# Performance work log

Hardware: AMD Instinct MI355X
Metric: run time of the kernel (lower is better)

The kernel has to match this reference:

```python
import jax, jax.numpy as jnp
import numpy as np

SCALE_POS = 2.0
SCALE_NEG = 40.0
THRESH_POS = 0.5
THRESH_NEG = 0.5
MARGIN = 0.1
EPS = 1e-5


def setup_inputs() -> dict:
    key = jax.random.key(0)
    kf, kl = jax.random.split(key)
    B, D, NUM_CLASSES = 4096, 1024, 64
    feats = jax.random.normal(kf, (B, D), dtype=jnp.float32)
    feats = feats / jnp.linalg.norm(feats, axis=1, keepdims=True)  # L2-normalized embeddings
    labels = jax.random.randint(kl, (B,), 0, NUM_CLASSES, dtype=jnp.int64)
    return {"feats": feats, "labels": labels}


def reference(feats, labels):
    B = feats.shape[0]
    sim = jnp.matmul(feats, feats.T)  # [B, B]
    same = labels[:, None] == labels[None, :]
    pos_mask = same & (sim < 1.0 - EPS)  # drop self / near-duplicate pairs
    neg_mask = ~same

    # hard mining: keep negatives above min positive - margin, positives below max negative + margin
    min_pos = jnp.min(jnp.where(pos_mask, sim, jnp.inf), axis=1)   # [B]
    max_neg = jnp.max(jnp.where(neg_mask, sim, -jnp.inf), axis=1)  # [B]
    neg_sel = neg_mask & (sim + MARGIN > min_pos[:, None])
    pos_sel = pos_mask & (sim - MARGIN < max_neg[:, None])

    pos_sum = jnp.sum(jnp.where(pos_sel, jnp.exp(-SCALE_POS * (sim - THRESH_POS)), 0.0), axis=1)
    neg_sum = jnp.sum(jnp.where(neg_sel, jnp.exp(SCALE_NEG * (sim - THRESH_NEG)), 0.0), axis=1)
    pos_loss = jnp.log1p(pos_sum) / SCALE_POS
    neg_loss = jnp.log1p(neg_sum) / SCALE_NEG

    valid = jnp.any(pos_sel, axis=1) & jnp.any(neg_sel, axis=1)  # rows skipped by original loop
    return jnp.sum(jnp.where(valid, pos_loss + neg_loss, 0.0)) / B
```

## Files before the change

kernel.cpp:

```cpp
#include <hip/hip_runtime.h>

typedef _Float16 half8 __attribute__((ext_vector_type(8)));
typedef float floatx4 __attribute__((ext_vector_type(4)));
typedef int intx4 __attribute__((ext_vector_type(4)));
typedef int intx8 __attribute__((ext_vector_type(8)));
typedef __attribute__((address_space(1))) const void gvoid;
typedef __attribute__((address_space(3))) void svoid;

#define SCALE_POS 2.0f
#define SCALE_NEG 40.0f
#define THRESH 0.5f
#define MARGIN 0.1f
#define EPSV 1e-5f

__global__ void k_init(const float* __restrict__ feats,
                       unsigned char* __restrict__ f8,
                       float* __restrict__ out,
                       int total4) {
    int i = blockIdx.x * blockDim.x + threadIdx.x;
    if (i < total4) {
        float4 v = ((const float4*)feats)[i];
        int w = 0;
        w = __builtin_amdgcn_cvt_pk_fp8_f32(v.x, v.y, w, false);
        w = __builtin_amdgcn_cvt_pk_fp8_f32(v.z, v.w, w, true);
        ((int*)f8)[i] = w;
    }
    if (i == 0) out[0] = 0.f;
}

__global__ void __launch_bounds__(256, 4)
k_gemm_h(const unsigned char* __restrict__ f8,
         const int* __restrict__ labels,
         float* __restrict__ pmin,
         float* __restrict__ pmax,
         _Float16* __restrict__ simh,
         int D, int nb) {
    __shared__ __align__(16) unsigned char As[128 * 128];
    __shared__ __align__(16) unsigned char Bs[128 * 128];
    __shared__ int labR[128], labC[128];

    const int Bsz = nb * 128;

    const int bid0 = blockIdx.x;
    const int t = (bid0 & 7) * 66 + (bid0 >> 3);
    int rb = 0, rem = t;
    while (rem >= nb - rb) { rem -= nb - rb; ++rb; }
    const int cb = rb + rem;
    const int rowBase = rb * 128;
    const int colBase = cb * 128;

    const int tid = threadIdx.x;
    const int lane = tid & 63;
    const int wave = tid >> 6;
    const int wr = wave >> 1;
    const int wc = wave & 1;
    const int q = lane >> 4;
    const int cIn = lane & 15;

    if (tid < 128) labR[tid] = labels[rowBase + tid];
    else           labC[tid - 128] = labels[colBase + (tid - 128)];

    const int subrow = lane >> 3;
    const int swz = (lane & 7) ^ subrow;
    const unsigned char* gP[8];
    unsigned char* lP[8];
#pragma unroll
    for (int j = 0; j < 8; ++j) {
        const int c = wave * 8 + j;
        const int grow = (c < 16) ? (rowBase + c * 8 + subrow)
                                  : (colBase + (c - 16) * 8 + subrow);
        gP[j] = f8 + (size_t)grow * D + swz * 16;
        lP[j] = ((c < 16) ? (As + c * 1024) : (Bs + (c - 16) * 1024)) + lane * 16;
    }

    int aOff0[4], aOff1[4], bOff0[4], bOff1[4];
#pragma unroll
    for (int i = 0; i < 4; ++i) {
        const int rA = wr * 64 + i * 16 + cIn;
        aOff0[i] = rA * 128 + ((2 * q) ^ (rA & 7)) * 16;
        aOff1[i] = rA * 128 + ((2 * q + 1) ^ (rA & 7)) * 16;
        const int rB = wc * 64 + i * 16 + cIn;
        bOff0[i] = rB * 128 + ((2 * q) ^ (rB & 7)) * 16;
        bOff1[i] = rB * 128 + ((2 * q + 1) ^ (rB & 7)) * 16;
    }

    floatx4 acc[4][4] = {};

    const int KT = D >> 7;
    for (int kt = 0; kt < KT; ++kt) {
        const int kOff = kt * 128;
        __syncthreads();
#pragma unroll
        for (int j = 0; j < 8; ++j)
            __builtin_amdgcn_global_load_lds((gvoid*)(gP[j] + kOff), (svoid*)lP[j], 16, 0, 0);
        __syncthreads();

        intx8 a[4], b[4];
#pragma unroll
        for (int i = 0; i < 4; ++i) {
            intx4 lo = *(const intx4*)(As + aOff0[i]);
            intx4 hi = *(const intx4*)(As + aOff1[i]);
            a[i] = __builtin_shufflevector(lo, hi, 0, 1, 2, 3, 4, 5, 6, 7);
        }
#pragma unroll
        for (int i = 0; i < 4; ++i) {
            intx4 lo = *(const intx4*)(Bs + bOff0[i]);
            intx4 hi = *(const intx4*)(Bs + bOff1[i]);
            b[i] = __builtin_shufflevector(lo, hi, 0, 1, 2, 3, 4, 5, 6, 7);
        }
#pragma unroll
        for (int i = 0; i < 4; ++i)
#pragma unroll
            for (int j2 = 0; j2 < 4; ++j2)
                acc[i][j2] = __builtin_amdgcn_mfma_scale_f32_16x16x128_f8f6f4(
                    a[i], b[j2], acc[i][j2], 0, 0,
                    0, 0x7f7f7f7f,
                    0, 0x7f7f7f7f);
    }

    int rLabv[16];
#pragma unroll
    for (int mi = 0; mi < 4; ++mi)
#pragma unroll
        for (int rr = 0; rr < 4; ++rr)
            rLabv[mi * 4 + rr] = labR[wr * 64 + mi * 16 + q * 4 + rr];
    int cLabv[4];
#pragma unroll
    for (int ni = 0; ni < 4; ++ni)
        cLabv[ni] = labC[wc * 64 + ni * 16 + cIn];

    {
        half8* dst = (half8*)(simh + (size_t)(2 * t + wc) * 8192
                                   + (size_t)(wr * 64 + lane) * 64);
#pragma unroll
        for (int mi = 0; mi < 4; ++mi) {
            half8 h0, h1;
#pragma unroll
            for (int ni = 0; ni < 2; ++ni)
#pragma unroll
                for (int rr = 0; rr < 4; ++rr) {
                    h0[ni * 4 + rr] = (_Float16)acc[mi][ni][rr];
                    h1[ni * 4 + rr] = (_Float16)acc[mi][ni + 2][rr];
                }
            dst[mi * 2] = h0;
            dst[mi * 2 + 1] = h1;
        }
    }

    {
        float* pmnRow = pmin + (size_t)(2 * cb + wc) * Bsz + rowBase;
        float* pmxRow = pmax + (size_t)(2 * cb + wc) * Bsz + rowBase;
#pragma unroll
        for (int mi = 0; mi < 4; ++mi)
#pragma unroll
            for (int rr = 0; rr < 4; ++rr) {
                const int rLoc = wr * 64 + mi * 16 + q * 4 + rr;
                const int rLab = rLabv[mi * 4 + rr];
                float vmin = 1e30f, vmax = -1e30f;
#pragma unroll
                for (int ni = 0; ni < 4; ++ni) {
                    float s = acc[mi][ni][rr];
                    if (rLab == cLabv[ni]) {
                        if (s < 1.0f - EPSV) vmin = fminf(vmin, s);
                    } else {
                        vmax = fmaxf(vmax, s);
                    }
                }
#pragma unroll
                for (int off = 8; off; off >>= 1) {
                    vmin = fminf(vmin, __shfl_xor(vmin, off, 16));
                    vmax = fmaxf(vmax, __shfl_xor(vmax, off, 16));
                }
                if (cIn == 0) {
                    pmnRow[rLoc] = vmin;
                    pmxRow[rLoc] = vmax;
                }
            }
    }

    if (rb != cb) {
        float* pmnCol = pmin + (size_t)(2 * rb + wr) * Bsz + colBase;
        float* pmxCol = pmax + (size_t)(2 * rb + wr) * Bsz + colBase;
#pragma unroll
        for (int ni = 0; ni < 4; ++ni) {
            const int cLab = cLabv[ni];
            float vmin = 1e30f, vmax = -1e30f;
#pragma unroll
            for (int mi = 0; mi < 4; ++mi)
#pragma unroll
                for (int rr = 0; rr < 4; ++rr) {
                    float s = acc[mi][ni][rr];
                    if (rLabv[mi * 4 + rr] == cLab) {
                        if (s < 1.0f - EPSV) vmin = fminf(vmin, s);
                    } else {
                        vmax = fmaxf(vmax, s);
                    }
                }
            vmin = fminf(vmin, __shfl_xor(vmin, 16, 64));
            vmin = fminf(vmin, __shfl_xor(vmin, 32, 64));
            vmax = fmaxf(vmax, __shfl_xor(vmax, 16, 64));
            vmax = fmaxf(vmax, __shfl_xor(vmax, 32, 64));
            if (q == 0) {
                const int cLoc = wc * 64 + ni * 16 + cIn;
                pmnCol[cLoc] = vmin;
                pmxCol[cLoc] = vmax;
            }
        }
    }
}

__global__ void __launch_bounds__(256)
k_sum2f(const _Float16* __restrict__ simh,
        const int* __restrict__ labels,
        const float* __restrict__ pmin,
        const float* __restrict__ pmax,
        float* __restrict__ psP, float* __restrict__ psN,
        int nb, int B) {
    __shared__ int labR[128], labC[128];
    __shared__ float gNR[128], gPR[128], gNC[128], gPC[128];

    int t = blockIdx.x;
    int rb = 0, rem = t;
    while (rem >= nb - rb) { rem -= nb - rb; ++rb; }
    const int cb = rb + rem;
    const int rowBase = rb * 128;

    const int tid = threadIdx.x;
    const int sub = tid >> 7;
    const int stid = tid & 127;
    const int wave = stid >> 6;
    const int lane = tid & 63;
    const int q = lane >> 4;
    const int cIn = lane & 15;
    const int colBase = cb * 128 + sub * 64;

    {
        const int j = tid & 127;
        const int base = (tid < 128) ? (rowBase + j) : (cb * 128 + j);
        float mn = 1e30f, mx = -1e30f;
#pragma unroll 4
        for (int k = 0; k < 64; ++k) {
            mn = fminf(mn, pmin[(size_t)k * B + base]);
            mx = fmaxf(mx, pmax[(size_t)k * B + base]);
        }
        if (tid < 128) {
            labR[j] = labels[rowBase + j];
            gNR[j] = mn - MARGIN;
            gPR[j] = mx + MARGIN;
        } else {
            labC[j] = labels[cb * 128 + j];
            gNC[j] = mn - MARGIN;
            gPC[j] = mx + MARGIN;
        }
    }
    __syncthreads();

    int cLabv[4];
    float gNCv[4], gPCv[4];
#pragma unroll
    for (int ni = 0; ni < 4; ++ni) {
        const int j = sub * 64 + ni * 16 + cIn;
        cLabv[ni] = labC[j];
        gNCv[ni] = gNC[j];
        gPCv[ni] = gPC[j];
    }

    const half8* src = (const half8*)(simh + (size_t)(2 * t + sub) * 8192 + (size_t)stid * 64);
    half8 hv[8];
#pragma unroll
    for (int v = 0; v < 8; ++v) hv[v] = src[v];

    float cps[4] = {}, cns[4] = {};
    const bool offd = (rb != cb);

    float* psPRow = psP + (size_t)(2 * cb + sub) * B + rowBase;
    float* psNRow = psN + (size_t)(2 * cb + sub) * B + rowBase;

#pragma unroll
    for (int mi = 0; mi < 4; ++mi)
#pragma unroll
        for (int rr = 0; rr < 4; ++rr) {
            const int rLoc = wave * 64 + mi * 16 + q * 4 + rr;
            const int rLab = labR[rLoc];
            const float gn = gNR[rLoc];
            const float gp = gPR[rLoc];
            float rp = 0.f, rn = 0.f;
#pragma unroll
            for (int ni = 0; ni < 4; ++ni) {
                const int idx = mi * 16 + ni * 4 + rr;
                const float s = (float)hv[idx >> 3][idx & 7];
                if (rLab == cLabv[ni]) {
                    if (s < 1.0f - EPSV) {
                        float ev = __expf(-SCALE_POS * (s - THRESH));
                        if (s < gp) rp += ev;
                        if (offd && s < gPCv[ni]) cps[ni] += ev;
                    }
                } else {
                    float ev = __expf(SCALE_NEG * (s - THRESH));
                    if (s > gn) rn += ev;
                    if (offd && s > gNCv[ni]) cns[ni] += ev;
                }
            }
#pragma unroll
            for (int off = 8; off; off >>= 1) {
                rp += __shfl_xor(rp, off, 16);
                rn += __shfl_xor(rn, off, 16);
            }
            if (cIn == 0) {
                psPRow[rLoc] = rp;
                psNRow[rLoc] = rn;
            }
        }
    if (offd) {
        float* psPCol = psP + (size_t)(2 * rb + wave) * B + colBase;
        float* psNCol = psN + (size_t)(2 * rb + wave) * B + colBase;
#pragma unroll
        for (int ni = 0; ni < 4; ++ni) {
            cps[ni] += __shfl_xor(cps[ni], 16, 64);
            cps[ni] += __shfl_xor(cps[ni], 32, 64);
            cns[ni] += __shfl_xor(cns[ni], 16, 64);
            cns[ni] += __shfl_xor(cns[ni], 32, 64);
            if (q == 0) {
                const int cLoc = ni * 16 + cIn;
                psPCol[cLoc] = cps[ni];
                psNCol[cLoc] = cns[ni];
            }
        }
    }
}

__global__ void __launch_bounds__(256)
k_final(const float* __restrict__ psP, const float* __restrict__ psN,
        float* __restrict__ out, int B) {
    __shared__ float red[4];
    const int r = blockIdx.x * 256 + threadIdx.x;
    float P = 0.f, N = 0.f;
    for (int k = 0; k < 64; ++k) {
        P += psP[(size_t)k * B + r];
        N += psN[(size_t)k * B + r];
    }
    float a = (P > 0.f && N > 0.f)
                  ? log1pf(P) * (1.0f / SCALE_POS) + log1pf(N) * (1.0f / SCALE_NEG)
                  : 0.f;
#pragma unroll
    for (int off = 32; off; off >>= 1) a += __shfl_down(a, off, 64);
    const int tid = threadIdx.x;
    if ((tid & 63) == 0) red[tid >> 6] = a;
    __syncthreads();
    if (tid == 0)
        atomicAdd(out, (red[0] + red[1] + red[2] + red[3]) / (float)B);
}

extern "C" void kernel_launch(void* const* d_in, const int* in_sizes, int n_in,
                              void* d_out, int out_size, void* d_ws, size_t ws_size,
                              hipStream_t stream) {
    const float* feats = (const float*)d_in[0];
    const int* labels = (const int*)d_in[1];
    const int B = in_sizes[1];
    const int D = in_sizes[0] / B;
    const int nb = B / 128;
    const int NT = nb * (nb + 1) / 2;
    const int total4 = B * D / 4;

    char* ws = (char*)d_ws;
    unsigned char* f8 = (unsigned char*)ws;
    size_t off = (size_t)B * D;
    float* pmin = (float*)(ws + off); off += (size_t)64 * B * 4;
    float* pmax = (float*)(ws + off); off += (size_t)64 * B * 4;
    float* psP  = (float*)(ws + off); off += (size_t)64 * B * 4;
    float* psN  = (float*)(ws + off); off += (size_t)64 * B * 4;
    _Float16* simh = (_Float16*)(ws + ((off + 255) & ~(size_t)255));
    float* outp = (float*)d_out;

    k_init<<<(total4 + 255) / 256, 256, 0, stream>>>(feats, f8, outp, total4);

    k_gemm_h<<<NT, 256, 0, stream>>>(f8, labels, pmin, pmax, simh, D, nb);

    k_sum2f<<<NT, 256, 0, stream>>>(simh, labels, pmin, pmax, psP, psN, nb, B);

    k_final<<<B / 256, 256, 0, stream>>>(psP, psN, outp, B);
}
```

Baseline: 134.7 us.

## Split GEMM tile across eight waves with 64x32 per-wave subtiles

The similarity GEMM block grows from four to eight waves, so each wave computes a 64x32 subtile instead of 64x64, halving accumulator registers and per-wave global-to-LDS loads. This aims to hide more latency through more concurrent waves. The partial min/max buffers double to 128 slices to match the finer column split. Because column-direction stats fill only some slots, k_init now pre-fills the buffers with sentinel values. The cost is extra init writes and twice as many partial reads in the reduction kernel.

Result: no change. 136.6 us (+1.4%).

```diff
diff --git a/kernel.cpp b/kernel.cpp
--- a/kernel.cpp
+++ b/kernel.cpp
@@ -15,8 +15,9 @@
 
 __global__ void k_init(const float* __restrict__ feats,
                        unsigned char* __restrict__ f8,
+                       float* __restrict__ pmin, float* __restrict__ pmax,
                        float* __restrict__ out,
-                       int total4) {
+                       int total4, int nstat) {
     int i = blockIdx.x * blockDim.x + threadIdx.x;
     if (i < total4) {
         float4 v = ((const float4*)feats)[i];
@@ -25,10 +26,14 @@
         w = __builtin_amdgcn_cvt_pk_fp8_f32(v.z, v.w, w, true);
         ((int*)f8)[i] = w;
     }
+    if (i < nstat) {
+        pmin[i] = 1e30f;
+        pmax[i] = -1e30f;
+    }
     if (i == 0) out[0] = 0.f;
 }
 
-__global__ void __launch_bounds__(256, 4)
+__global__ void __launch_bounds__(512, 4)
 k_gemm_h(const unsigned char* __restrict__ f8,
          const int* __restrict__ labels,
          float* __restrict__ pmin,
@@ -52,50 +57,53 @@
     const int tid = threadIdx.x;
     const int lane = tid & 63;
     const int wave = tid >> 6;
-    const int wr = wave >> 1;
-    const int wc = wave & 1;
+    const int wr = wave >> 2;
+    const int wc4 = wave & 3;
     const int q = lane >> 4;
     const int cIn = lane & 15;
 
     if (tid < 128) labR[tid] = labels[rowBase + tid];
-    else           labC[tid - 128] = labels[colBase + (tid - 128)];
+    else if (tid < 256) labC[tid - 128] = labels[colBase + (tid - 128)];
 
     const int subrow = lane >> 3;
     const int swz = (lane & 7) ^ subrow;
-    const unsigned char* gP[8];
-    unsigned char* lP[8];
-#pragma unroll
-    for (int j = 0; j < 8; ++j) {
-        const int c = wave * 8 + j;
+    const unsigned char* gP[4];
+    unsigned char* lP[4];
+#pragma unroll
+    for (int j = 0; j < 4; ++j) {
+        const int c = wave * 4 + j;
         const int grow = (c < 16) ? (rowBase + c * 8 + subrow)
                                   : (colBase + (c - 16) * 8 + subrow);
         gP[j] = f8 + (size_t)grow * D + swz * 16;
         lP[j] = ((c < 16) ? (As + c * 1024) : (Bs + (c - 16) * 1024)) + lane * 16;
     }
 
-    int aOff0[4], aOff1[4], bOff0[4], bOff1[4];
+    int aOff0[4], aOff1[4], bOff0[2], bOff1[2];
 #pragma unroll
     for (int i = 0; i < 4; ++i) {
         const int rA = wr * 64 + i * 16 + cIn;
         aOff0[i] = rA * 128 + ((2 * q) ^ (rA & 7)) * 16;
         aOff1[i] = rA * 128 + ((2 * q + 1) ^ (rA & 7)) * 16;
-        const int rB = wc * 64 + i * 16 + cIn;
+    }
+#pragma unroll
+    for (int i = 0; i < 2; ++i) {
+        const int rB = wc4 * 32 + i * 16 + cIn;
         bOff0[i] = rB * 128 + ((2 * q) ^ (rB & 7)) * 16;
         bOff1[i] = rB * 128 + ((2 * q + 1) ^ (rB & 7)) * 16;
     }
 
-    floatx4 acc[4][4] = {};
+    floatx4 acc[4][2] = {};
 
     const int KT = D >> 7;
     for (int kt = 0; kt < KT; ++kt) {
         const int kOff = kt * 128;
         __syncthreads();
 #pragma unroll
-        for (int j = 0; j < 8; ++j)
+        for (int j = 0; j < 4; ++j)
             __builtin_amdgcn_global_load_lds((gvoid*)(gP[j] + kOff), (svoid*)lP[j], 16, 0, 0);
         __syncthreads();
 
-        intx8 a[4], b[4];
+        intx8 a[4], b[2];
 #pragma unroll
         for (int i = 0; i < 4; ++i) {
             intx4 lo = *(const intx4*)(As + aOff0[i]);
@@ -103,7 +111,7 @@
             a[i] = __builtin_shufflevector(lo, hi, 0, 1, 2, 3, 4, 5, 6, 7);
         }
 #pragma unroll
-        for (int i = 0; i < 4; ++i) {
+        for (int i = 0; i < 2; ++i) {
             intx4 lo = *(const intx4*)(Bs + bOff0[i]);
             intx4 hi = *(const intx4*)(Bs + bOff1[i]);
             b[i] = __builtin_shufflevector(lo, hi, 0, 1, 2, 3, 4, 5, 6, 7);
@@ -111,7 +119,7 @@
 #pragma unroll
         for (int i = 0; i < 4; ++i)
 #pragma unroll
-            for (int j2 = 0; j2 < 4; ++j2)
+            for (int j2 = 0; j2 < 2; ++j2)
                 acc[i][j2] = __builtin_amdgcn_mfma_scale_f32_16x16x128_f8f6f4(
                     a[i], b[j2], acc[i][j2], 0, 0,
                     0, 0x7f7f7f7f,
@@ -124,32 +132,29 @@
 #pragma unroll
         for (int rr = 0; rr < 4; ++rr)
             rLabv[mi * 4 + rr] = labR[wr * 64 + mi * 16 + q * 4 + rr];
-    int cLabv[4];
-#pragma unroll
-    for (int ni = 0; ni < 4; ++ni)
-        cLabv[ni] = labC[wc * 64 + ni * 16 + cIn];
+    int cLabv[2];
+#pragma unroll
+    for (int ni = 0; ni < 2; ++ni)
+        cLabv[ni] = labC[wc4 * 32 + ni * 16 + cIn];
 
     {
-        half8* dst = (half8*)(simh + (size_t)(2 * t + wc) * 8192
+        half8* dst = (half8*)(simh + (size_t)(2 * t + (wc4 >> 1)) * 8192
                                    + (size_t)(wr * 64 + lane) * 64);
 #pragma unroll
         for (int mi = 0; mi < 4; ++mi) {
-            half8 h0, h1;
+            half8 h0;
 #pragma unroll
             for (int ni = 0; ni < 2; ++ni)
 #pragma unroll
-                for (int rr = 0; rr < 4; ++rr) {
+                for (int rr = 0; rr < 4; ++rr)
                     h0[ni * 4 + rr] = (_Float16)acc[mi][ni][rr];
-                    h1[ni * 4 + rr] = (_Float16)acc[mi][ni + 2][rr];
-                }
-            dst[mi * 2] = h0;
-            dst[mi * 2 + 1] = h1;
+            dst[mi * 2 + (wc4 & 1)] = h0;
         }
     }
 
     {
-        float* pmnRow = pmin + (size_t)(2 * cb + wc) * Bsz + rowBase;
-        float* pmxRow = pmax + (size_t)(2 * cb + wc) * Bsz + rowBase;
+        float* pmnRow = pmin + (size_t)(4 * cb + wc4) * Bsz + rowBase;
+        float* pmxRow = pmax + (size_t)(4 * cb + wc4) * Bsz + rowBase;
 #pragma unroll
         for (int mi = 0; mi < 4; ++mi)
 #pragma unroll
@@ -158,7 +163,7 @@
                 const int rLab = rLabv[mi * 4 + rr];
                 float vmin = 1e30f, vmax = -1e30f;
 #pragma unroll
-                for (int ni = 0; ni < 4; ++ni) {
+                for (int ni = 0; ni < 2; ++ni) {
                     float s = acc[mi][ni][rr];
                     if (rLab == cLabv[ni]) {
                         if (s < 1.0f - EPSV) vmin = fminf(vmin, s);
@@ -179,10 +184,10 @@
     }
 
     if (rb != cb) {
-        float* pmnCol = pmin + (size_t)(2 * rb + wr) * Bsz + colBase;
-        float* pmxCol = pmax + (size_t)(2 * rb + wr) * Bsz + colBase;
-#pragma unroll
-        for (int ni = 0; ni < 4; ++ni) {
+        float* pmnCol = pmin + (size_t)(4 * rb + wr) * Bsz + colBase;
+        float* pmxCol = pmax + (size_t)(4 * rb + wr) * Bsz + colBase;
+#pragma unroll
+        for (int ni = 0; ni < 2; ++ni) {
             const int cLab = cLabv[ni];
             float vmin = 1e30f, vmax = -1e30f;
 #pragma unroll
@@ -201,7 +206,7 @@
             vmax = fmaxf(vmax, __shfl_xor(vmax, 16, 64));
             vmax = fmaxf(vmax, __shfl_xor(vmax, 32, 64));
             if (q == 0) {
-                const int cLoc = wc * 64 + ni * 16 + cIn;
+                const int cLoc = wc4 * 32 + ni * 16 + cIn;
                 pmnCol[cLoc] = vmin;
                 pmxCol[cLoc] = vmax;
             }
@@ -239,7 +244,7 @@
         const int base = (tid < 128) ? (rowBase + j) : (cb * 128 + j);
         float mn = 1e30f, mx = -1e30f;
 #pragma unroll 4
-        for (int k = 0; k < 64; ++k) {
+        for (int k = 0; k < 128; ++k) {
             mn = fminf(mn, pmin[(size_t)k * B + base]);
             mx = fmaxf(mx, pmax[(size_t)k * B + base]);
         }
@@ -361,20 +366,22 @@
     const int nb = B / 128;
     const int NT = nb * (nb + 1) / 2;
     const int total4 = B * D / 4;
+    const int nstat = 128 * B;
 
     char* ws = (char*)d_ws;
     unsigned char* f8 = (unsigned char*)ws;
     size_t off = (size_t)B * D;
-    float* pmin = (float*)(ws + off); off += (size_t)64 * B * 4;
-    float* pmax = (float*)(ws + off); off += (size_t)64 * B * 4;
+    float* pmin = (float*)(ws + off); off += (size_t)128 * B * 4;
+    float* pmax = (float*)(ws + off); off += (size_t)128 * B * 4;
     float* psP  = (float*)(ws + off); off += (size_t)64 * B * 4;
     float* psN  = (float*)(ws + off); off += (size_t)64 * B * 4;
     _Float16* simh = (_Float16*)(ws + ((off + 255) & ~(size_t)255));
     float* outp = (float*)d_out;
 
-    k_init<<<(total4 + 255) / 256, 256, 0, stream>>>(feats, f8, outp, total4);
-
-    k_gemm_h<<<NT, 256, 0, stream>>>(f8, labels, pmin, pmax, simh, D, nb);
+    k_init<<<(total4 + 255) / 256, 256, 0, stream>>>(feats, f8, pmin, pmax,
+                                                     outp, total4, nstat);
+
+    k_gemm_h<<<NT, 512, 0, stream>>>(f8, labels, pmin, pmax, simh, D, nb);
 
     k_sum2f<<<NT, 256, 0, stream>>>(simh, labels, pmin, pmax, psP, psN, nb, B);
 
```

## Fuse fp32-to-fp8 conversion into GEMM tile loads, drop init kernel

Applied to the files above, without the earlier changes.

Removes the separate conversion kernel. The GEMM now reads fp32 features directly, converts them to fp8 in registers and writes them into swizzled LDS, and zeroing the output moves into block 0. This drops a launch and the fp8 round trip through global memory. In exchange every tile reads 4x more bytes from global memory and loses the async global-to-LDS path, and launch bounds change from 4 to 2 waves per SIMD.

New measurement: 165.8 us. +23.1%, slower.

```diff
diff --git a/kernel.cpp b/kernel.cpp
--- a/kernel.cpp
+++ b/kernel.cpp
@@ -4,8 +4,6 @@
 typedef float floatx4 __attribute__((ext_vector_type(4)));
 typedef int intx4 __attribute__((ext_vector_type(4)));
 typedef int intx8 __attribute__((ext_vector_type(8)));
-typedef __attribute__((address_space(1))) const void gvoid;
-typedef __attribute__((address_space(3))) void svoid;
 
 #define SCALE_POS 2.0f
 #define SCALE_NEG 40.0f
@@ -13,27 +11,13 @@
 #define MARGIN 0.1f
 #define EPSV 1e-5f
 
-__global__ void k_init(const float* __restrict__ feats,
-                       unsigned char* __restrict__ f8,
-                       float* __restrict__ out,
-                       int total4) {
-    int i = blockIdx.x * blockDim.x + threadIdx.x;
-    if (i < total4) {
-        float4 v = ((const float4*)feats)[i];
-        int w = 0;
-        w = __builtin_amdgcn_cvt_pk_fp8_f32(v.x, v.y, w, false);
-        w = __builtin_amdgcn_cvt_pk_fp8_f32(v.z, v.w, w, true);
-        ((int*)f8)[i] = w;
-    }
-    if (i == 0) out[0] = 0.f;
-}
-
-__global__ void __launch_bounds__(256, 4)
-k_gemm_h(const unsigned char* __restrict__ f8,
+__global__ void __launch_bounds__(256, 2)
+k_gemm_h(const float* __restrict__ feats,
          const int* __restrict__ labels,
          float* __restrict__ pmin,
          float* __restrict__ pmax,
          _Float16* __restrict__ simh,
+         float* __restrict__ out,
          int D, int nb) {
     __shared__ __align__(16) unsigned char As[128 * 128];
     __shared__ __align__(16) unsigned char Bs[128 * 128];
@@ -57,20 +41,22 @@
     const int q = lane >> 4;
     const int cIn = lane & 15;
 
+    if (bid0 == 0 && tid == 0) out[0] = 0.f;
+
     if (tid < 128) labR[tid] = labels[rowBase + tid];
     else           labC[tid - 128] = labels[colBase + (tid - 128)];
 
     const int subrow = lane >> 3;
-    const int swz = (lane & 7) ^ subrow;
-    const unsigned char* gP[8];
-    unsigned char* lP[8];
+    const int blk = lane & 7;
+    const float* gF[8];
+    int wOff[8];
 #pragma unroll
     for (int j = 0; j < 8; ++j) {
         const int c = wave * 8 + j;
         const int grow = (c < 16) ? (rowBase + c * 8 + subrow)
                                   : (colBase + (c - 16) * 8 + subrow);
-        gP[j] = f8 + (size_t)grow * D + swz * 16;
-        lP[j] = ((c < 16) ? (As + c * 1024) : (Bs + (c - 16) * 1024)) + lane * 16;
+        gF[j] = feats + (size_t)grow * D + blk * 16;
+        wOff[j] = c * 1024 + subrow * 128 + ((blk ^ subrow) << 4);
     }
 
     int aOff0[4], aOff1[4], bOff0[4], bOff1[4];
@@ -88,11 +74,23 @@
 
     const int KT = D >> 7;
     for (int kt = 0; kt < KT; ++kt) {
-        const int kOff = kt * 128;
         __syncthreads();
 #pragma unroll
-        for (int j = 0; j < 8; ++j)
-            __builtin_amdgcn_global_load_lds((gvoid*)(gP[j] + kOff), (svoid*)lP[j], 16, 0, 0);
+        for (int j = 0; j < 8; ++j) {
+            const floatx4* sp = (const floatx4*)(gF[j] + kt * 128);
+            floatx4 f0 = sp[0], f1 = sp[1], f2 = sp[2], f3 = sp[3];
+            int w0 = 0, w1 = 0, w2 = 0, w3 = 0;
+            w0 = __builtin_amdgcn_cvt_pk_fp8_f32(f0[0], f0[1], w0, false);
+            w0 = __builtin_amdgcn_cvt_pk_fp8_f32(f0[2], f0[3], w0, true);
+            w1 = __builtin_amdgcn_cvt_pk_fp8_f32(f1[0], f1[1], w1, false);
+            w1 = __builtin_amdgcn_cvt_pk_fp8_f32(f1[2], f1[3], w1, true);
+            w2 = __builtin_amdgcn_cvt_pk_fp8_f32(f2[0], f2[1], w2, false);
+            w2 = __builtin_amdgcn_cvt_pk_fp8_f32(f2[2], f2[3], w2, true);
+            w3 = __builtin_amdgcn_cvt_pk_fp8_f32(f3[0], f3[1], w3, false);
+            w3 = __builtin_amdgcn_cvt_pk_fp8_f32(f3[2], f3[3], w3, true);
+            intx4 v = {w0, w1, w2, w3};
+            *(intx4*)(((wOff[j] < 16384) ? As : (Bs - 16384)) + wOff[j]) = v;
+        }
         __syncthreads();
 
         intx8 a[4], b[4];
@@ -360,11 +358,9 @@
     const int D = in_sizes[0] / B;
     const int nb = B / 128;
     const int NT = nb * (nb + 1) / 2;
-    const int total4 = B * D / 4;
 
     char* ws = (char*)d_ws;
-    unsigned char* f8 = (unsigned char*)ws;
-    size_t off = (size_t)B * D;
+    size_t off = 0;
     float* pmin = (float*)(ws + off); off += (size_t)64 * B * 4;
     float* pmax = (float*)(ws + off); off += (size_t)64 * B * 4;
     float* psP  = (float*)(ws + off); off += (size_t)64 * B * 4;
@@ -372,9 +368,7 @@
     _Float16* simh = (_Float16*)(ws + ((off + 255) & ~(size_t)255));
     float* outp = (float*)d_out;
 
-    k_init<<<(total4 + 255) / 256, 256, 0, stream>>>(feats, f8, outp, total4);
-
-    k_gemm_h<<<NT, 256, 0, stream>>>(f8, labels, pmin, pmax, simh, D, nb);
+    k_gemm_h<<<NT, 256, 0, stream>>>(feats, labels, pmin, pmax, simh, outp, D, nb);
 
     k_sum2f<<<NT, 256, 0, stream>>>(simh, labels, pmin, pmax, psP, psN, nb, B);
 
```
